# Kernel tuning notes

Measured on AMD Instinct MI355X. Metric: run time of the kernel, lower is better.

The kernel has to match this reference:

```python
import jax, jax.numpy as jnp
import numpy as np

B, T, D = 16, 4096, 1024
NUM_CLASSES = 1000
K, TOP_M = 4, 8
TEMP, EPS = 0.07, 1e-6


def setup_inputs() -> dict:
    key = jax.random.key(0)
    k_e, k_v, k_w = jax.random.split(key, 3)
    E = jax.random.normal(k_e, (B, T, D), dtype=jnp.float32)
    v = jax.random.normal(k_v, (K, D), dtype=jnp.float32) * 0.02
    m_logits = jnp.zeros((K, D), dtype=jnp.float32)
    cls_W = jax.random.normal(k_w, (K, NUM_CLASSES, D), dtype=jnp.float32) * (1.0 / D ** 0.5)
    cls_b = jnp.zeros((K, NUM_CLASSES), dtype=jnp.float32)
    beta = jnp.ones((K,), dtype=jnp.float32)
    alpha = jnp.ones((K,), dtype=jnp.float32)
    return {"E": E, "v": v, "m_logits": m_logits, "cls_W": cls_W,
            "cls_b": cls_b, "beta": beta, "alpha": alpha}


def reference(E, v, m_logits, cls_W, cls_b, beta, alpha):
    tokens = E  # (B, T, D)
    logits_sum = jnp.zeros((E.shape[0], cls_W.shape[1]), dtype=E.dtype)
    top_m = min(TOP_M, E.shape[1])
    for k in range(K):
        # unit peel direction u_k
        vk = v[k] * jax.nn.sigmoid(m_logits[k])          # (D,)
        u = vk / (jnp.linalg.norm(vk) + EPS)             # (D,)
        # token scores and soft attention
        coeff_all = jnp.einsum('btd,d->bt', tokens, u)   # (B, T) = E @ u
        scores = coeff_all / TEMP
        att = jax.nn.softmax(scores, axis=1)             # (B, T)
        # hard top-m tokens
        _, top_idx = jax.lax.top_k(scores, top_m)        # (B, m)
        top_tokens = jnp.take_along_axis(tokens, top_idx[:, :, None], axis=1)  # (B, m, D)
        # rank-1 projections onto u: proj(X) = (X@u)[...,None]*u
        coeff_top = jnp.einsum('bmd,d->bm', top_tokens, u)
        z_hard = jnp.sum(coeff_top, axis=1)[:, None] * u           # (B, D)
        z_soft = jnp.sum(coeff_all * att, axis=1)[:, None] * u     # (B, D)
        z_k = 0.5 * (z_hard + z_soft)
        logits_k = z_k @ cls_W[k].T + cls_b[k]                      # (B, C)
        logits_sum = logits_sum + alpha[k] * logits_k
        # residual peel: remove u component from all tokens
        tokens = tokens - beta[k] * (coeff_all[:, :, None] * u)
    return logits_sum
```

## Files before the change

### kernel.cpp

```cpp
#include <hip/hip_runtime.h>
#include <math.h>

#define DD 1024
#define TT 4096
#define BB 16
#define KK 4
#define CC 1000
#define TEMP_F 0.07f
#define EPS_F 1e-6f
#define NPROJ 2048

#define CE(a, b) { float _mx = fmaxf(a, b), _mn = fminf(a, b); a = _mx; b = _mn; }
#define INS8(y_) { float y = (y_); \
    CE(s0, y) CE(s1, y) CE(s2, y) CE(s3, y) CE(s4, y) CE(s5, y) CE(s6, y) CE(s7, y) }
#define RESORT8() { \
    CE(s0, s4) CE(s1, s5) CE(s2, s6) CE(s3, s7) \
    CE(s0, s2) CE(s1, s3) CE(s4, s6) CE(s5, s7) \
    CE(s0, s1) CE(s2, s3) CE(s4, s5) CE(s6, s7) }
#define WMERGE(off) { \
    float t0 = __shfl_xor(s0, off), t1 = __shfl_xor(s1, off), \
          t2 = __shfl_xor(s2, off), t3 = __shfl_xor(s3, off), \
          t4 = __shfl_xor(s4, off), t5 = __shfl_xor(s5, off), \
          t6 = __shfl_xor(s6, off), t7 = __shfl_xor(s7, off); \
    s0 = fmaxf(s0, t7); s1 = fmaxf(s1, t6); s2 = fmaxf(s2, t5); s3 = fmaxf(s3, t4); \
    s4 = fmaxf(s4, t3); s5 = fmaxf(s5, t2); s6 = fmaxf(s6, t1); s7 = fmaxf(s7, t0); \
    RESORT8() }

__global__ __launch_bounds__(256) void k_main(const float* __restrict__ E,
                                              const float* __restrict__ W,
                                              const float* __restrict__ v,
                                              const float* __restrict__ m,
                                              const float* __restrict__ beta,
                                              float* __restrict__ c0,
                                              float* __restrict__ wdot) {
    __shared__ float u_lds[KK * DD];
    __shared__ float G_lds[6];
    int tid = threadIdx.x, w = tid >> 6, lane = tid & 63;

    {
        float s_reg[16];
        float ss = 0.f;
#pragma unroll
        for (int i = 0; i < 16; ++i) {
            int d = lane + i * 64;
            float mv = m[w * DD + d];
            float s = v[w * DD + d] * (1.f / (1.f + expf(-mv)));
            s_reg[i] = s; ss += s * s;
        }
#pragma unroll
        for (int off = 32; off; off >>= 1) ss += __shfl_xor(ss, off);
        float inv = 1.f / (sqrtf(ss) + EPS_F);
#pragma unroll
        for (int i = 0; i < 16; ++i) u_lds[w * DD + lane + i * 64] = s_reg[i] * inv;
    }
    __syncthreads();
    for (int p = w; p < 6; p += 4) {
        int j = (p < 3) ? 0 : ((p < 5) ? 1 : 2);
        int k = (p < 3) ? (p + 1) : ((p < 5) ? (p - 1) : 3);
        float acc = 0.f;
#pragma unroll
        for (int i = 0; i < 16; ++i) {
            int d = lane + i * 64;
            acc += u_lds[j * DD + d] * u_lds[k * DD + d];
        }
#pragma unroll
        for (int off = 32; off; off >>= 1) acc += __shfl_xor(acc, off);
        if (lane == 0) G_lds[p] = acc;
    }
    __syncthreads();

    if (blockIdx.x < NPROJ) {
        float g01 = G_lds[0], g02 = G_lds[1], g03 = G_lds[2];
        float g12 = G_lds[3], g13 = G_lds[4], g23 = G_lds[5];
        float b0 = beta[0], b1 = beta[1], b2 = beta[2];
        float4 U[KK][4];
#pragma unroll
        for (int k = 0; k < KK; ++k)
#pragma unroll
            for (int j = 0; j < 4; ++j)
                U[k][j] = *reinterpret_cast<const float4*>(u_lds + k * DD + lane * 4 + j * 256);
        const int ITERS = (BB * TT) / (NPROJ * 4);
#pragma unroll 1
        for (int it = 0; it < ITERS; ++it) {
            size_t g = (size_t)(blockIdx.x * 4 + w) + (size_t)it * (NPROJ * 4);
            const float* e = E + g * DD;
            float a0 = 0.f, a1 = 0.f, a2 = 0.f, a3 = 0.f;
#pragma unroll
            for (int j = 0; j < 4; ++j) {
                float4 ev = *reinterpret_cast<const float4*>(e + lane * 4 + j * 256);
                a0 += ev.x * U[0][j].x + ev.y * U[0][j].y + ev.z * U[0][j].z + ev.w * U[0][j].w;
                a1 += ev.x * U[1][j].x + ev.y * U[1][j].y + ev.z * U[1][j].z + ev.w * U[1][j].w;
                a2 += ev.x * U[2][j].x + ev.y * U[2][j].y + ev.z * U[2][j].z + ev.w * U[2][j].w;
                a3 += ev.x * U[3][j].x + ev.y * U[3][j].y + ev.z * U[3][j].z + ev.w * U[3][j].w;
            }
#pragma unroll
            for (int off = 32; off; off >>= 1) {
                a0 += __shfl_xor(a0, off);
                a1 += __shfl_xor(a1, off);
                a2 += __shfl_xor(a2, off);
                a3 += __shfl_xor(a3, off);
            }
            float f0 = a0;
            float f1 = a1 - b0 * g01 * f0;
            float f2 = a2 - b0 * g02 * f0 - b1 * g12 * f1;
            float f3 = a3 - b0 * g03 * f0 - b1 * g13 * f1 - b2 * g23 * f2;
            if (lane == 0)
                *reinterpret_cast<float4*>(c0 + g * 4) = make_float4(f0, f1, f2, f3);
        }
    } else {
        int c = blockIdx.x - NPROJ;
        const float* wr = W + ((size_t)w * CC + c) * DD;
        float acc = 0.f;
#pragma unroll
        for (int j = 0; j < 4; ++j) {
            float4 wv = *reinterpret_cast<const float4*>(wr + lane * 4 + j * 256);
            float4 uv = *reinterpret_cast<const float4*>(u_lds + w * DD + lane * 4 + j * 256);
            acc += wv.x * uv.x + wv.y * uv.y + wv.z * uv.z + wv.w * uv.w;
        }
#pragma unroll
        for (int off = 32; off; off >>= 1) acc += __shfl_xor(acc, off);
        if (lane == 0) wdot[w * CC + c] = acc;
    }
}

__global__ __launch_bounds__(256) void k_peel_out(const float* __restrict__ c0,
                                                  const float* __restrict__ wdot,
                                                  const float* __restrict__ bias,
                                                  const float* __restrict__ alpha,
                                                  float* __restrict__ out) {
    __shared__ float csc[KK];
    int tid = threadIdx.x, w = tid >> 6, lane = tid & 63;
    int b = blockIdx.x;
    float fk[64];
    float mx = -INFINITY;
#pragma unroll
    for (int i = 0; i < 64; ++i) {
        int t = lane + i * 64;
        float4 cv = *reinterpret_cast<const float4*>(c0 + ((size_t)b * TT + t) * 4);
        float f = (w == 0) ? cv.x : ((w == 1) ? cv.y : ((w == 2) ? cv.z : cv.w));
        fk[i] = f; mx = fmaxf(mx, f);
    }
#pragma unroll
    for (int off = 32; off; off >>= 1) mx = fmaxf(mx, __shfl_xor(mx, off));
    const float invT = 1.f / TEMP_F;
    float se = 0.f, sce = 0.f;
#pragma unroll
    for (int i = 0; i < 64; ++i) {
        float e = expf((fk[i] - mx) * invT);
        se += e; sce += fk[i] * e;
    }
#pragma unroll
    for (int off = 32; off; off >>= 1) {
        se += __shfl_xor(se, off);
        sce += __shfl_xor(sce, off);
    }
    float zsoft = sce / se;
    float s0 = -INFINITY, s1 = -INFINITY, s2 = -INFINITY, s3 = -INFINITY,
          s4 = -INFINITY, s5 = -INFINITY, s6 = -INFINITY, s7 = -INFINITY;
#pragma unroll
    for (int i = 0; i < 64; ++i) INS8(fk[i]);
    WMERGE(1) WMERGE(2) WMERGE(4) WMERGE(8) WMERGE(16) WMERGE(32)
    if (lane == 0) {
        float sumtop = s0 + s1 + s2 + s3 + s4 + s5 + s6 + s7;
        csc[w] = 0.5f * (sumtop + zsoft);
    }
    __syncthreads();
    float al0 = alpha[0], al1 = alpha[1], al2 = alpha[2], al3 = alpha[3];
    float c0s = csc[0], c1s = csc[1], c2s = csc[2], c3s = csc[3];
    for (int c = tid; c < CC; c += 256) {
        float s = al0 * (c0s * wdot[0 * CC + c] + bias[0 * CC + c])
                + al1 * (c1s * wdot[1 * CC + c] + bias[1 * CC + c])
                + al2 * (c2s * wdot[2 * CC + c] + bias[2 * CC + c])
                + al3 * (c3s * wdot[3 * CC + c] + bias[3 * CC + c]);
        out[(size_t)b * CC + c] = s;
    }
}

extern "C" void kernel_launch(void* const* d_in, const int* in_sizes, int n_in,
                              void* d_out, int out_size, void* d_ws, size_t ws_size,
                              hipStream_t stream) {
    const float* E     = (const float*)d_in[0];
    const float* v     = (const float*)d_in[1];
    const float* m     = (const float*)d_in[2];
    const float* W     = (const float*)d_in[3];
    const float* cb    = (const float*)d_in[4];
    const float* beta  = (const float*)d_in[5];
    const float* alpha = (const float*)d_in[6];
    float* out = (float*)d_out;
    float* ws = (float*)d_ws;

    float* wdot = ws;
    float* c0   = ws + 4096;

    k_main<<<NPROJ + CC, 256, 0, stream>>>(E, W, v, m, beta, c0, wdot);
    k_peel_out<<<BB, 256, 0, stream>>>(c0, wdot, cb, alpha, out);
}
```

Measured before the change: 72.13 us.

## Defer u normalization and Gram correction from main kernel to output kernel

Result: slower. 81.57 us (+13.1%).

```diff
diff --git a/kernel.cpp b/kernel.cpp
--- a/kernel.cpp
+++ b/kernel.cpp
@@ -26,59 +26,32 @@
     s4 = fmaxf(s4, t3); s5 = fmaxf(s5, t2); s6 = fmaxf(s6, t1); s7 = fmaxf(s7, t0); \
     RESORT8() }
 
+__device__ __forceinline__ float4 sigw4(const float* __restrict__ v,
+                                        const float* __restrict__ m, int off) {
+    float4 vv = *reinterpret_cast<const float4*>(v + off);
+    float4 mm = *reinterpret_cast<const float4*>(m + off);
+    float4 r;
+    r.x = vv.x * (1.f / (1.f + expf(-mm.x)));
+    r.y = vv.y * (1.f / (1.f + expf(-mm.y)));
+    r.z = vv.z * (1.f / (1.f + expf(-mm.z)));
+    r.w = vv.w * (1.f / (1.f + expf(-mm.w)));
+    return r;
+}
+
 __global__ __launch_bounds__(256) void k_main(const float* __restrict__ E,
                                               const float* __restrict__ W,
                                               const float* __restrict__ v,
                                               const float* __restrict__ m,
-                                              const float* __restrict__ beta,
                                               float* __restrict__ c0,
-                                              float* __restrict__ wdot) {
-    __shared__ float u_lds[KK * DD];
-    __shared__ float G_lds[6];
+                                              float* __restrict__ wraw) {
     int tid = threadIdx.x, w = tid >> 6, lane = tid & 63;
-
-    {
-        float s_reg[16];
-        float ss = 0.f;
-#pragma unroll
-        for (int i = 0; i < 16; ++i) {
-            int d = lane + i * 64;
-            float mv = m[w * DD + d];
-            float s = v[w * DD + d] * (1.f / (1.f + expf(-mv)));
-            s_reg[i] = s; ss += s * s;
-        }
-#pragma unroll
-        for (int off = 32; off; off >>= 1) ss += __shfl_xor(ss, off);
-        float inv = 1.f / (sqrtf(ss) + EPS_F);
-#pragma unroll
-        for (int i = 0; i < 16; ++i) u_lds[w * DD + lane + i * 64] = s_reg[i] * inv;
-    }
-    __syncthreads();
-    for (int p = w; p < 6; p += 4) {
-        int j = (p < 3) ? 0 : ((p < 5) ? 1 : 2);
-        int k = (p < 3) ? (p + 1) : ((p < 5) ? (p - 1) : 3);
-        float acc = 0.f;
-#pragma unroll
-        for (int i = 0; i < 16; ++i) {
-            int d = lane + i * 64;
-            acc += u_lds[j * DD + d] * u_lds[k * DD + d];
-        }
-#pragma unroll
-        for (int off = 32; off; off >>= 1) acc += __shfl_xor(acc, off);
-        if (lane == 0) G_lds[p] = acc;
-    }
-    __syncthreads();
-
     if (blockIdx.x < NPROJ) {
-        float g01 = G_lds[0], g02 = G_lds[1], g03 = G_lds[2];
-        float g12 = G_lds[3], g13 = G_lds[4], g23 = G_lds[5];
-        float b0 = beta[0], b1 = beta[1], b2 = beta[2];
-        float4 U[KK][4];
+        float4 S[KK][4];
 #pragma unroll
         for (int k = 0; k < KK; ++k)
 #pragma unroll
             for (int j = 0; j < 4; ++j)
-                U[k][j] = *reinterpret_cast<const float4*>(u_lds + k * DD + lane * 4 + j * 256);
+                S[k][j] = sigw4(v, m, k * DD + lane * 4 + j * 256);
         const int ITERS = (BB * TT) / (NPROJ * 4);
 #pragma unroll 1
         for (int it = 0; it < ITERS; ++it) {
@@ -88,10 +61,10 @@
 #pragma unroll
             for (int j = 0; j < 4; ++j) {
                 float4 ev = *reinterpret_cast<const float4*>(e + lane * 4 + j * 256);
-                a0 += ev.x * U[0][j].x + ev.y * U[0][j].y + ev.z * U[0][j].z + ev.w * U[0][j].w;
-                a1 += ev.x * U[1][j].x + ev.y * U[1][j].y + ev.z * U[1][j].z + ev.w * U[1][j].w;
-                a2 += ev.x * U[2][j].x + ev.y * U[2][j].y + ev.z * U[2][j].z + ev.w * U[2][j].w;
-                a3 += ev.x * U[3][j].x + ev.y * U[3][j].y + ev.z * U[3][j].z + ev.w * U[3][j].w;
+                a0 += ev.x * S[0][j].x + ev.y * S[0][j].y + ev.z * S[0][j].z + ev.w * S[0][j].w;
+                a1 += ev.x * S[1][j].x + ev.y * S[1][j].y + ev.z * S[1][j].z + ev.w * S[1][j].w;
+                a2 += ev.x * S[2][j].x + ev.y * S[2][j].y + ev.z * S[2][j].z + ev.w * S[2][j].w;
+                a3 += ev.x * S[3][j].x + ev.y * S[3][j].y + ev.z * S[3][j].z + ev.w * S[3][j].w;
             }
 #pragma unroll
             for (int off = 32; off; off >>= 1) {
@@ -100,44 +73,79 @@
                 a2 += __shfl_xor(a2, off);
                 a3 += __shfl_xor(a3, off);
             }
-            float f0 = a0;
-            float f1 = a1 - b0 * g01 * f0;
-            float f2 = a2 - b0 * g02 * f0 - b1 * g12 * f1;
-            float f3 = a3 - b0 * g03 * f0 - b1 * g13 * f1 - b2 * g23 * f2;
             if (lane == 0)
-                *reinterpret_cast<float4*>(c0 + g * 4) = make_float4(f0, f1, f2, f3);
+                *reinterpret_cast<float4*>(c0 + g * 4) = make_float4(a0, a1, a2, a3);
         }
     } else {
         int c = blockIdx.x - NPROJ;
+        float4 S4[4];
+#pragma unroll
+        for (int j = 0; j < 4; ++j)
+            S4[j] = sigw4(v, m, w * DD + lane * 4 + j * 256);
         const float* wr = W + ((size_t)w * CC + c) * DD;
         float acc = 0.f;
 #pragma unroll
         for (int j = 0; j < 4; ++j) {
             float4 wv = *reinterpret_cast<const float4*>(wr + lane * 4 + j * 256);
-            float4 uv = *reinterpret_cast<const float4*>(u_lds + w * DD + lane * 4 + j * 256);
-            acc += wv.x * uv.x + wv.y * uv.y + wv.z * uv.z + wv.w * uv.w;
+            acc += wv.x * S4[j].x + wv.y * S4[j].y + wv.z * S4[j].z + wv.w * S4[j].w;
         }
 #pragma unroll
         for (int off = 32; off; off >>= 1) acc += __shfl_xor(acc, off);
-        if (lane == 0) wdot[w * CC + c] = acc;
+        if (lane == 0) wraw[w * CC + c] = acc;
     }
 }
 
 __global__ __launch_bounds__(256) void k_peel_out(const float* __restrict__ c0,
-                                                  const float* __restrict__ wdot,
+                                                  const float* __restrict__ wraw,
+                                                  const float* __restrict__ v,
+                                                  const float* __restrict__ m,
+                                                  const float* __restrict__ beta,
                                                   const float* __restrict__ bias,
                                                   const float* __restrict__ alpha,
                                                   float* __restrict__ out) {
+    __shared__ float red[10];
     __shared__ float csc[KK];
     int tid = threadIdx.x, w = tid >> 6, lane = tid & 63;
     int b = blockIdx.x;
+    static const int PJ[10] = {0, 1, 2, 3, 0, 0, 0, 1, 1, 2};
+    static const int PK[10] = {0, 1, 2, 3, 1, 2, 3, 2, 3, 3};
+#pragma unroll 1
+    for (int p = w; p < 10; p += 4) {
+        int j = PJ[p], k = PK[p];
+        float acc = 0.f;
+#pragma unroll
+        for (int i = 0; i < 16; ++i) {
+            int d = lane + i * 64;
+            float sj = v[j * DD + d] * (1.f / (1.f + expf(-m[j * DD + d])));
+            float sk = (j == k) ? sj
+                                : v[k * DD + d] * (1.f / (1.f + expf(-m[k * DD + d])));
+            acc += sj * sk;
+        }
+#pragma unroll
+        for (int off = 32; off; off >>= 1) acc += __shfl_xor(acc, off);
+        if (lane == 0) red[p] = acc;
+    }
+    __syncthreads();
+    float inv0 = 1.f / (sqrtf(red[0]) + EPS_F);
+    float inv1 = 1.f / (sqrtf(red[1]) + EPS_F);
+    float inv2 = 1.f / (sqrtf(red[2]) + EPS_F);
+    float inv3 = 1.f / (sqrtf(red[3]) + EPS_F);
+    float g01 = red[4] * inv0 * inv1, g02 = red[5] * inv0 * inv2,
+          g03 = red[6] * inv0 * inv3, g12 = red[7] * inv1 * inv2,
+          g13 = red[8] * inv1 * inv3, g23 = red[9] * inv2 * inv3;
+    float b0 = beta[0], b1 = beta[1], b2 = beta[2];
+
     float fk[64];
     float mx = -INFINITY;
 #pragma unroll
     for (int i = 0; i < 64; ++i) {
         int t = lane + i * 64;
         float4 cv = *reinterpret_cast<const float4*>(c0 + ((size_t)b * TT + t) * 4);
-        float f = (w == 0) ? cv.x : ((w == 1) ? cv.y : ((w == 2) ? cv.z : cv.w));
+        float f0 = cv.x * inv0;
+        float f1 = cv.y * inv1 - b0 * g01 * f0;
+        float f2 = cv.z * inv2 - b0 * g02 * f0 - b1 * g12 * f1;
+        float f3 = cv.w * inv3 - b0 * g03 * f0 - b1 * g13 * f1 - b2 * g23 * f2;
+        float f = (w == 0) ? f0 : ((w == 1) ? f1 : ((w == 2) ? f2 : f3));
         fk[i] = f; mx = fmaxf(mx, f);
     }
 #pragma unroll
@@ -166,12 +174,13 @@
     }
     __syncthreads();
     float al0 = alpha[0], al1 = alpha[1], al2 = alpha[2], al3 = alpha[3];
-    float c0s = csc[0], c1s = csc[1], c2s = csc[2], c3s = csc[3];
+    float c0s = csc[0] * inv0, c1s = csc[1] * inv1,
+          c2s = csc[2] * inv2, c3s = csc[3] * inv3;
     for (int c = tid; c < CC; c += 256) {
-        float s = al0 * (c0s * wdot[0 * CC + c] + bias[0 * CC + c])
-                + al1 * (c1s * wdot[1 * CC + c] + bias[1 * CC + c])
-                + al2 * (c2s * wdot[2 * CC + c] + bias[2 * CC + c])
-                + al3 * (c3s * wdot[3 * CC + c] + bias[3 * CC + c]);
+        float s = al0 * (c0s * wraw[0 * CC + c] + bias[0 * CC + c])
+                + al1 * (c1s * wraw[1 * CC + c] + bias[1 * CC + c])
+                + al2 * (c2s * wraw[2 * CC + c] + bias[2 * CC + c])
+                + al3 * (c3s * wraw[3 * CC + c] + bias[3 * CC + c]);
         out[(size_t)b * CC + c] = s;
     }
 }
@@ -189,9 +198,9 @@
     float* out = (float*)d_out;
     float* ws = (float*)d_ws;
 
-    float* wdot = ws;
+    float* wraw = ws;
     float* c0   = ws + 4096;
 
-    k_main<<<NPROJ + CC, 256, 0, stream>>>(E, W, v, m, beta, c0, wdot);
-    k_peel_out<<<BB, 256, 0, stream>>>(c0, wdot, cb, alpha, out);
-}
+    k_main<<<NPROJ + CC, 256, 0, stream>>>(E, W, v, m, c0, wraw);
+    k_peel_out<<<BB, 256, 0, stream>>>(c0, wraw, v, m, beta, cb, alpha, out);
+}
```

## Hoist direction setup into a separate kernel and software-pipeline E loads

Applied to the files above, without the earlier changes.

Result: faster. 63.09 us (-12.5%).

```diff
diff --git a/kernel.cpp b/kernel.cpp
--- a/kernel.cpp
+++ b/kernel.cpp
@@ -9,6 +9,8 @@
 #define TEMP_F 0.07f
 #define EPS_F 1e-6f
 #define NPROJ 2048
+#define SWEEP (NPROJ * 4)
+#define ITERS ((BB * TT) / SWEEP)
 
 #define CE(a, b) { float _mx = fmaxf(a, b), _mn = fminf(a, b); a = _mx; b = _mn; }
 #define INS8(y_) { float y = (y_); \
@@ -26,32 +28,30 @@
     s4 = fmaxf(s4, t3); s5 = fmaxf(s5, t2); s6 = fmaxf(s6, t1); s7 = fmaxf(s7, t0); \
     RESORT8() }
 
-__global__ __launch_bounds__(256) void k_main(const float* __restrict__ E,
-                                              const float* __restrict__ W,
-                                              const float* __restrict__ v,
-                                              const float* __restrict__ m,
-                                              const float* __restrict__ beta,
-                                              float* __restrict__ c0,
-                                              float* __restrict__ wdot) {
+__global__ __launch_bounds__(256) void k_u_g(const float* __restrict__ v,
+                                             const float* __restrict__ m,
+                                             float* __restrict__ u_ws,
+                                             float* __restrict__ G_ws) {
     __shared__ float u_lds[KK * DD];
-    __shared__ float G_lds[6];
     int tid = threadIdx.x, w = tid >> 6, lane = tid & 63;
-
-    {
-        float s_reg[16];
-        float ss = 0.f;
-#pragma unroll
-        for (int i = 0; i < 16; ++i) {
-            int d = lane + i * 64;
-            float mv = m[w * DD + d];
-            float s = v[w * DD + d] * (1.f / (1.f + expf(-mv)));
-            s_reg[i] = s; ss += s * s;
-        }
-#pragma unroll
-        for (int off = 32; off; off >>= 1) ss += __shfl_xor(ss, off);
-        float inv = 1.f / (sqrtf(ss) + EPS_F);
-#pragma unroll
-        for (int i = 0; i < 16; ++i) u_lds[w * DD + lane + i * 64] = s_reg[i] * inv;
+    float s_reg[16];
+    float ss = 0.f;
+#pragma unroll
+    for (int i = 0; i < 16; ++i) {
+        int d = lane + i * 64;
+        float mv = m[w * DD + d];
+        float s = v[w * DD + d] * (1.f / (1.f + expf(-mv)));
+        s_reg[i] = s; ss += s * s;
+    }
+#pragma unroll
+    for (int off = 32; off; off >>= 1) ss += __shfl_xor(ss, off);
+    float inv = 1.f / (sqrtf(ss) + EPS_F);
+#pragma unroll
+    for (int i = 0; i < 16; ++i) {
+        int d = lane + i * 64;
+        float uu = s_reg[i] * inv;
+        u_lds[w * DD + d] = uu;
+        u_ws[w * DD + d] = uu;
     }
     __syncthreads();
     for (int p = w; p < 6; p += 4) {
@@ -65,33 +65,43 @@
         }
 #pragma unroll
         for (int off = 32; off; off >>= 1) acc += __shfl_xor(acc, off);
-        if (lane == 0) G_lds[p] = acc;
-    }
-    __syncthreads();
-
+        if (lane == 0) G_ws[p] = acc;
+    }
+}
+
+__global__ __launch_bounds__(256) void k_proj_wu(const float* __restrict__ E,
+                                                 const float* __restrict__ W,
+                                                 const float* __restrict__ u_ws,
+                                                 float* __restrict__ c0,
+                                                 float* __restrict__ wdot) {
+    int tid = threadIdx.x, w = tid >> 6, lane = tid & 63;
     if (blockIdx.x < NPROJ) {
-        float g01 = G_lds[0], g02 = G_lds[1], g03 = G_lds[2];
-        float g12 = G_lds[3], g13 = G_lds[4], g23 = G_lds[5];
-        float b0 = beta[0], b1 = beta[1], b2 = beta[2];
         float4 U[KK][4];
 #pragma unroll
         for (int k = 0; k < KK; ++k)
 #pragma unroll
             for (int j = 0; j < 4; ++j)
-                U[k][j] = *reinterpret_cast<const float4*>(u_lds + k * DD + lane * 4 + j * 256);
-        const int ITERS = (BB * TT) / (NPROJ * 4);
+                U[k][j] = *reinterpret_cast<const float4*>(u_ws + k * DD + lane * 4 + j * 256);
+        size_t base = (size_t)(blockIdx.x * 4 + w);
+        const float* e0 = E + base * DD + lane * 4;
+        float4 ev[4];
+#pragma unroll
+        for (int j = 0; j < 4; ++j)
+            ev[j] = *reinterpret_cast<const float4*>(e0 + j * 256);
 #pragma unroll 1
-        for (int it = 0; it < ITERS; ++it) {
-            size_t g = (size_t)(blockIdx.x * 4 + w) + (size_t)it * (NPROJ * 4);
-            const float* e = E + g * DD;
+        for (int it = 0; it < ITERS - 1; ++it) {
+            const float* en = e0 + (size_t)(it + 1) * ((size_t)SWEEP * DD);
+            float4 evn[4];
+#pragma unroll
+            for (int j = 0; j < 4; ++j)
+                evn[j] = *reinterpret_cast<const float4*>(en + j * 256);
             float a0 = 0.f, a1 = 0.f, a2 = 0.f, a3 = 0.f;
 #pragma unroll
             for (int j = 0; j < 4; ++j) {
-                float4 ev = *reinterpret_cast<const float4*>(e + lane * 4 + j * 256);
-                a0 += ev.x * U[0][j].x + ev.y * U[0][j].y + ev.z * U[0][j].z + ev.w * U[0][j].w;
-                a1 += ev.x * U[1][j].x + ev.y * U[1][j].y + ev.z * U[1][j].z + ev.w * U[1][j].w;
-                a2 += ev.x * U[2][j].x + ev.y * U[2][j].y + ev.z * U[2][j].z + ev.w * U[2][j].w;
-                a3 += ev.x * U[3][j].x + ev.y * U[3][j].y + ev.z * U[3][j].z + ev.w * U[3][j].w;
+                a0 += ev[j].x * U[0][j].x + ev[j].y * U[0][j].y + ev[j].z * U[0][j].z + ev[j].w * U[0][j].w;
+                a1 += ev[j].x * U[1][j].x + ev[j].y * U[1][j].y + ev[j].z * U[1][j].z + ev[j].w * U[1][j].w;
+                a2 += ev[j].x * U[2][j].x + ev[j].y * U[2][j].y + ev[j].z * U[2][j].z + ev[j].w * U[2][j].w;
+                a3 += ev[j].x * U[3][j].x + ev[j].y * U[3][j].y + ev[j].z * U[3][j].z + ev[j].w * U[3][j].w;
             }
 #pragma unroll
             for (int off = 32; off; off >>= 1) {
@@ -100,21 +110,41 @@
                 a2 += __shfl_xor(a2, off);
                 a3 += __shfl_xor(a3, off);
             }
-            float f0 = a0;
-            float f1 = a1 - b0 * g01 * f0;
-            float f2 = a2 - b0 * g02 * f0 - b1 * g12 * f1;
-            float f3 = a3 - b0 * g03 * f0 - b1 * g13 * f1 - b2 * g23 * f2;
             if (lane == 0)
-                *reinterpret_cast<float4*>(c0 + g * 4) = make_float4(f0, f1, f2, f3);
+                *reinterpret_cast<float4*>(c0 + (base + (size_t)it * SWEEP) * 4) =
+                    make_float4(a0, a1, a2, a3);
+#pragma unroll
+            for (int j = 0; j < 4; ++j) ev[j] = evn[j];
+        }
+        {
+            float a0 = 0.f, a1 = 0.f, a2 = 0.f, a3 = 0.f;
+#pragma unroll
+            for (int j = 0; j < 4; ++j) {
+                a0 += ev[j].x * U[0][j].x + ev[j].y * U[0][j].y + ev[j].z * U[0][j].z + ev[j].w * U[0][j].w;
+                a1 += ev[j].x * U[1][j].x + ev[j].y * U[1][j].y + ev[j].z * U[1][j].z + ev[j].w * U[1][j].w;
+                a2 += ev[j].x * U[2][j].x + ev[j].y * U[2][j].y + ev[j].z * U[2][j].z + ev[j].w * U[2][j].w;
+                a3 += ev[j].x * U[3][j].x + ev[j].y * U[3][j].y + ev[j].z * U[3][j].z + ev[j].w * U[3][j].w;
+            }
+#pragma unroll
+            for (int off = 32; off; off >>= 1) {
+                a0 += __shfl_xor(a0, off);
+                a1 += __shfl_xor(a1, off);
+                a2 += __shfl_xor(a2, off);
+                a3 += __shfl_xor(a3, off);
+            }
+            if (lane == 0)
+                *reinterpret_cast<float4*>(c0 + (base + (size_t)(ITERS - 1) * SWEEP) * 4) =
+                    make_float4(a0, a1, a2, a3);
         }
     } else {
         int c = blockIdx.x - NPROJ;
         const float* wr = W + ((size_t)w * CC + c) * DD;
+        const float* ur = u_ws + w * DD;
         float acc = 0.f;
 #pragma unroll
         for (int j = 0; j < 4; ++j) {
             float4 wv = *reinterpret_cast<const float4*>(wr + lane * 4 + j * 256);
-            float4 uv = *reinterpret_cast<const float4*>(u_lds + w * DD + lane * 4 + j * 256);
+            float4 uv = *reinterpret_cast<const float4*>(ur + lane * 4 + j * 256);
             acc += wv.x * uv.x + wv.y * uv.y + wv.z * uv.z + wv.w * uv.w;
         }
 #pragma unroll
@@ -124,6 +154,8 @@
 }
 
 __global__ __launch_bounds__(256) void k_peel_out(const float* __restrict__ c0,
+                                                  const float* __restrict__ G_ws,
+                                                  const float* __restrict__ beta,
                                                   const float* __restrict__ wdot,
                                                   const float* __restrict__ bias,
                                                   const float* __restrict__ alpha,
@@ -131,13 +163,20 @@
     __shared__ float csc[KK];
     int tid = threadIdx.x, w = tid >> 6, lane = tid & 63;
     int b = blockIdx.x;
+    float g01 = G_ws[0], g02 = G_ws[1], g03 = G_ws[2];
+    float g12 = G_ws[3], g13 = G_ws[4], g23 = G_ws[5];
+    float b0 = beta[0], b1 = beta[1], b2 = beta[2];
     float fk[64];
     float mx = -INFINITY;
 #pragma unroll
     for (int i = 0; i < 64; ++i) {
         int t = lane + i * 64;
         float4 cv = *reinterpret_cast<const float4*>(c0 + ((size_t)b * TT + t) * 4);
-        float f = (w == 0) ? cv.x : ((w == 1) ? cv.y : ((w == 2) ? cv.z : cv.w));
+        float f0 = cv.x;
+        float f1 = cv.y - b0 * g01 * f0;
+        float f2 = cv.z - b0 * g02 * f0 - b1 * g12 * f1;
+        float f3 = cv.w - b0 * g03 * f0 - b1 * g13 * f1 - b2 * g23 * f2;
+        float f = (w == 0) ? f0 : ((w == 1) ? f1 : ((w == 2) ? f2 : f3));
         fk[i] = f; mx = fmaxf(mx, f);
     }
 #pragma unroll
@@ -189,9 +228,12 @@
     float* out = (float*)d_out;
     float* ws = (float*)d_ws;
 
-    float* wdot = ws;
-    float* c0   = ws + 4096;
-
-    k_main<<<NPROJ + CC, 256, 0, stream>>>(E, W, v, m, beta, c0, wdot);
-    k_peel_out<<<BB, 256, 0, stream>>>(c0, wdot, cb, alpha, out);
-}
+    float* u_ws = ws;
+    float* G_ws = ws + 4096;
+    float* wdot = ws + 4112;
+    float* c0   = ws + 8192;
+
+    k_u_g<<<1, 256, 0, stream>>>(v, m, u_ws, G_ws);
+    k_proj_wu<<<NPROJ + CC, 256, 0, stream>>>(E, W, u_ws, c0, wdot);
+    k_peel_out<<<BB, 256, 0, stream>>>(c0, G_ws, beta, wdot, cb, alpha, out);
+}
```
